# Performance work log

Measured on AMD Instinct MI355X. Metric: run time of the kernel, lower is better.

The kernel has to match this reference:

```python
import jax, jax.numpy as jnp
import numpy as np

TEMP = 1.75   # temp_schedule(epoch=5, warmup=10): 2.5 - 1.5*0.5
ALPHA = 0.5   # blend_schedule(epoch=5): 0.2 + 0.6*0.5
EPS = 1e-5
HEADS = 2


def _ln(x, g, b):
    mu = x.mean(-1, keepdims=True)
    var = ((x - mu) ** 2).mean(-1, keepdims=True)
    return (x - mu) * jax.lax.rsqrt(var + EPS) * g + b


def _gelu(x):
    return jax.nn.gelu(x, approximate=False)  # torch nn.GELU default = exact erf


def _attn_pool(x, ln_g, ln_b, in_w, in_b, out_w, out_b):
    # x: [N, T, E]; nn.MultiheadAttention self-attention then mean over T
    N, T, E = x.shape
    Dh = E // HEADS
    xn = _ln(x, ln_g, ln_b)
    qkv = xn @ in_w + in_b                      # [N, T, 3E] (in_w stored [E, 3E])
    q, k, v = jnp.split(qkv, 3, axis=-1)
    q = q.reshape(N, T, HEADS, Dh).transpose(0, 2, 1, 3)
    k = k.reshape(N, T, HEADS, Dh).transpose(0, 2, 1, 3)
    v = v.reshape(N, T, HEADS, Dh).transpose(0, 2, 1, 3)
    scores = jnp.einsum('nhqd,nhkd->nhqk', q, k) / jnp.sqrt(jnp.float32(Dh))
    a = jax.nn.softmax(scores, axis=-1)
    o = jnp.einsum('nhqk,nhkd->nhqd', a, v).transpose(0, 2, 1, 3).reshape(N, T, E)
    o = o @ out_w + out_b                       # [N, T, E]
    return o.mean(axis=1)                       # [N, E]


def setup_inputs() -> dict:
    key = jax.random.key(0)
    ks = iter(jax.random.split(key, 40))
    B, L, T, D = 4, 24, 400, 1024
    H = D // 2  # 512
    G = 4       # groups
    s = 0.02
    r = lambda shp: jax.random.normal(next(ks), shp, dtype=jnp.float32) * s
    inp = {
        'x': jax.random.normal(next(ks), (B, L, T, D), dtype=jnp.float32),
        'mlp_alpha': jnp.ones((L,), jnp.float32),
        # shared MLP: LN -> Linear(D,H) -> GELU -> Linear(H,H)
        's_ln_g': jnp.ones((D,), jnp.float32), 's_ln_b': jnp.zeros((D,), jnp.float32),
        's_w1': r((D, H)), 's_b1': jnp.zeros((H,), jnp.float32),
        's_w2': r((H, H)), 's_b2': jnp.zeros((H,), jnp.float32),
        # 4 group MLPs (stacked)
        'g_ln_g': jnp.ones((G, D), jnp.float32), 'g_ln_b': jnp.zeros((G, D), jnp.float32),
        'g_w1': r((G, D, H)), 'g_b1': jnp.zeros((G, H), jnp.float32),
        'g_w2': r((G, H, H)), 'g_b2': jnp.zeros((G, H), jnp.float32),
        # TimeAttentionPool (shared module): LN + MHA(512, 2 heads) + out_proj
        'p_ln_g': jnp.ones((H,), jnp.float32), 'p_ln_b': jnp.zeros((H,), jnp.float32),
        'p_in_w': r((H, 3 * H)), 'p_in_b': jnp.zeros((3 * H,), jnp.float32),
        'p_out_w': r((H, H)), 'p_out_b': jnp.zeros((H,), jnp.float32),
        # router: Linear(512,128) -> GELU -> Linear(128,1) -> sigmoid(/temp)
        'r_w1': r((H, 128)), 'r_b1': jnp.zeros((128,), jnp.float32),
        'r_w2': r((128, 1)), 'r_b2': jnp.zeros((1,), jnp.float32),
        # post norms
        'pn_g': jnp.ones((H,), jnp.float32), 'pn_b': jnp.zeros((H,), jnp.float32),
        'pnf_g': jnp.ones((H,), jnp.float32), 'pnf_b': jnp.zeros((H,), jnp.float32),
        # classifier 512 -> 256 -> 128 -> 2
        'c_w1': r((H, H // 2)), 'c_b1': jnp.zeros((H // 2,), jnp.float32),
        'c_w2': r((H // 2, H // 4)), 'c_b2': jnp.zeros((H // 4,), jnp.float32),
        'c_w3': r((H // 4, 2)), 'c_b3': jnp.zeros((2,), jnp.float32),
    }
    return inp


def reference(x, mlp_alpha, s_ln_g, s_ln_b, s_w1, s_b1, s_w2, s_b2,
              g_ln_g, g_ln_b, g_w1, g_b1, g_w2, g_b2,
              p_ln_g, p_ln_b, p_in_w, p_in_b, p_out_w, p_out_b,
              r_w1, r_b1, r_w2, r_b2, pn_g, pn_b, pnf_g, pnf_b,
              c_w1, c_b1, c_w2, c_b2, c_w3, c_b3):
    B, L, T, D = x.shape
    G = g_w1.shape[0]
    S = L // G  # group_size = 6; expert i uses group i // S
    H = s_w1.shape[1]

    # shared MLP over all experts at once (dropout inactive in eval)
    xs = _ln(x, s_ln_g, s_ln_b)                              # [B,L,T,D]
    shared = _gelu(xs @ s_w1 + s_b1) @ s_w2 + s_b2           # [B,L,T,H]

    # group MLPs: experts i//S -> group; reshape L -> (G, S)
    xg = x.reshape(B, G, S, T, D)
    xgn = _ln(xg, g_ln_g[:, None, None, :], g_ln_b[:, None, None, :])
    hg = _gelu(jnp.einsum('bgstd,gdh->bgsth', xgn, g_w1) + g_b1[None, :, None, None, :])
    grp = jnp.einsum('bgsth,ghk->bgstk', hg, g_w2) + g_b2[None, :, None, None, :]
    grp = grp.reshape(B, L, T, H)

    weighted = shared + mlp_alpha[None, :, None, None] * grp  # [B,L,T,H]

    # attn-pool every expert stream (fold L into batch)
    time_pooled = _attn_pool(weighted.reshape(B * L, T, H),
                             p_ln_g, p_ln_b, p_in_w, p_in_b, p_out_w, p_out_b)
    time_pooled = time_pooled.reshape(B, L, H)               # [B,L,H]

    # router
    rh = _gelu(time_pooled @ r_w1 + r_b1)
    logits_r = (rh @ r_w2 + r_b2)[..., 0]                    # [B,L]
    learned = jax.nn.sigmoid(logits_r / TEMP)
    routing_weights = ALPHA * learned + (1.0 - ALPHA) / L

    # soft fusion over experts
    fusion = (weighted * routing_weights[:, :, None, None]).sum(axis=1)  # [B,T,H]
    fusion = _ln(fusion, pn_g, pn_b).mean(axis=1)            # [B,H]

    shared_mean = shared.mean(axis=1)                        # [B,T,H]
    time_ctx = _attn_pool(shared_mean, p_ln_g, p_ln_b, p_in_w, p_in_b, p_out_w, p_out_b)

    fused_all = _ln(fusion, pnf_g, pnf_b) + _ln(time_ctx, pnf_g, pnf_b)  # [B,H]

    h = _gelu(fused_all @ c_w1 + c_b1)
    h = _gelu(h @ c_w2 + c_b2)
    logits = h @ c_w3 + c_b3                                 # [B,2]
    return logits, routing_weights, fused_all, time_pooled
```

## Files before the change

### kernel.cpp

```cpp
#include <hip/hip_runtime.h>
#include <stdint.h>


typedef float f32x4 __attribute__((ext_vector_type(4)));
typedef short bf16x8 __attribute__((ext_vector_type(8)));

__device__ __forceinline__ float bf2f(unsigned short u) {
  return __uint_as_float(((unsigned int)u) << 16);
}
__device__ __forceinline__ unsigned short f2bf(float f) {
  unsigned int u = __float_as_uint(f);
  u += 0x7fffu + ((u >> 16) & 1u);
  return (unsigned short)(u >> 16);
}
__device__ __forceinline__ float erf_fast(float x) {
  const float ax = fabsf(x);
  const float t = 1.0f / fmaf(0.3275911f, ax, 1.0f);
  float p = fmaf(1.061405429f, t, -1.453152027f);
  p = fmaf(p, t, 1.421413741f);
  p = fmaf(p, t, -0.284496736f);
  p = fmaf(p, t, 0.254829592f);
  const float e = __expf(-ax * ax);
  const float r = 1.0f - p * t * e;
  return copysignf(r, x);
}
__device__ __forceinline__ float gelu_f(float x) {
  return 0.5f * x * (1.0f + erf_fast(x * 0.70710678118654752440f));
}

typedef __attribute__((address_space(1))) const unsigned int gas_u32;
typedef __attribute__((address_space(3))) unsigned int las_u32;
__device__ __forceinline__ void gload16(const unsigned short* g, unsigned short* l) {
  __builtin_amdgcn_global_load_lds((gas_u32*)g, (las_u32*)l, 16, 0, 0);
}

template <int EPI, int GROUPED>
__global__ __launch_bounds__(256, 4) void gemm_bt(
    const unsigned short* __restrict__ A, const unsigned short* __restrict__ WT,
    const float* __restrict__ bias, unsigned short* __restrict__ Cout,
    const unsigned short* __restrict__ WT2, const float* __restrict__ bias2,
    const float* __restrict__ alpha_vec, unsigned short* __restrict__ vtbuf, int K,
    int N, int ldout, int Mslice) {
  const int tid = (int)threadIdx.x;
  const int w = tid >> 6, lane = tid & 63, g = lane >> 4, ql = lane & 15;
  const int wr = w >> 1, wc = w & 1;

  int bm, bn, z = 0;
  if (!GROUPED) {
    const int nbm = (int)gridDim.x, nbn = (int)gridDim.y;
    const int nb = nbm * nbn;
    const int lin = (int)blockIdx.x + nbm * (int)blockIdx.y;
    const int q = nb >> 3, r8 = nb & 7;
    const int xcd = lin & 7, c = lin >> 3;
    const int base = (xcd < r8) ? xcd * (q + 1) : r8 * (q + 1) + (xcd - r8) * q;
    const int widx = base + c;
    bm = widx / nbn;
    bn = widx - bm * nbn;
  } else {
    const int nbm = (int)gridDim.x, nbn = (int)gridDim.y;
    const int per_z = nbm * nbn;
    const int nb = per_z * (int)gridDim.z;
    const int lin =
        (int)blockIdx.x + nbm * ((int)blockIdx.y + (int)gridDim.y * (int)blockIdx.z);
    const int q = nb >> 3, r8 = nb & 7;
    const int xcd = lin & 7, c = lin >> 3;
    const int base = (xcd < r8) ? xcd * (q + 1) : r8 * (q + 1) + (xcd - r8) * q;
    const int widx = base + c;
    z = widx / per_z;
    const int rem = widx - z * per_z;
    bm = rem / nbn;
    bn = rem - bm * nbn;
  }
  const int n0 = bn * 128;

  int rowbase, rows_here;
  int nw0 = n0;
  const unsigned short* wt = WT;
  const float* bs = bias;
  if (GROUPED) {
    const int grp = z & 3;
    rowbase = z * Mslice + bm * 128;
    rows_here = Mslice - bm * 128;
    if (rows_here > 128) rows_here = 128;
    if (EPI == 4) {
      if (bn >= 4) {
        wt = WT2 + (size_t)grp * 512 * (size_t)K;
        bs = bias2 + (size_t)grp * 512;
        nw0 = n0 - 512;
      }
    } else if (EPI == 5) {
      wt = WT + (size_t)grp * (size_t)N * (size_t)K;
    } else {
      wt = WT + (size_t)grp * (size_t)N * (size_t)K;
      bs = bias + (size_t)grp * (size_t)N;
    }
  } else {
    rowbase = bm * 128;
    rows_here = Mslice - bm * 128;
    if (rows_here > 128) rows_here = 128;
  }

  __shared__ __align__(16) unsigned short sA[2][128 * 32];
  __shared__ __align__(16) unsigned short sB[2][128 * 32];

  f32x4 acc[4][4];
#pragma unroll
  for (int i = 0; i < 4; ++i)
#pragma unroll
    for (int j = 0; j < 4; ++j) acc[i][j] = (f32x4){0.f, 0.f, 0.f, 0.f};

  const int swzg = (lane & 3) ^ ((lane >> 3) & 3);
  const int rA0 = w * 32 + (lane >> 2);
  const int rA1 = rA0 + 16;
  const int rA0c = rA0 < rows_here ? rA0 : rows_here - 1;
  const int rA1c = rA1 < rows_here ? rA1 : rows_here - 1;
  const unsigned short* a0p = A + (size_t)(rowbase + rA0c) * K + swzg * 8;
  const unsigned short* a1p = A + (size_t)(rowbase + rA1c) * K + swzg * 8;
  const unsigned short* b0p = wt + (size_t)(nw0 + rA0) * K + swzg * 8;
  const unsigned short* b1p = wt + (size_t)(nw0 + rA1) * K + swzg * 8;
  const int ldsw = w * 1024;

  const int aroff = (wr * 64 + ql) * 32 + ((g ^ ((ql >> 1) & 3)) * 8);
  const int broff = (wc * 64 + ql) * 32 + ((g ^ ((ql >> 1) & 3)) * 8);

  const int nsteps = K >> 5;
  gload16(a0p, &sA[0][ldsw]);
  gload16(a1p, &sA[0][ldsw + 512]);
  gload16(b0p, &sB[0][ldsw]);
  gload16(b1p, &sB[0][ldsw + 512]);
  __syncthreads();

  for (int s = 0; s < nsteps; ++s) {
    const int cur = s & 1;
    if (s + 1 < nsteps) {
      const int k0 = (s + 1) << 5;
      const int nxt = cur ^ 1;
      gload16(a0p + k0, &sA[nxt][ldsw]);
      gload16(a1p + k0, &sA[nxt][ldsw + 512]);
      gload16(b0p + k0, &sB[nxt][ldsw]);
      gload16(b1p + k0, &sB[nxt][ldsw + 512]);
    }
    bf16x8 af[4], bfr[4];
#pragma unroll
    for (int mi = 0; mi < 4; ++mi)
      af[mi] = *(const bf16x8*)(&sA[cur][aroff + mi * 512]);
#pragma unroll
    for (int ni = 0; ni < 4; ++ni)
      bfr[ni] = *(const bf16x8*)(&sB[cur][broff + ni * 512]);
#pragma unroll
    for (int mi = 0; mi < 4; ++mi)
#pragma unroll
      for (int ni = 0; ni < 4; ++ni)
        acc[mi][ni] =
            __builtin_amdgcn_mfma_f32_16x16x32_bf16(af[mi], bfr[ni], acc[mi][ni], 0, 0, 0);
    __syncthreads();
  }

#pragma unroll
  for (int mi = 0; mi < 4; ++mi) {
#pragma unroll
    for (int r = 0; r < 4; ++r) {
      const int rloc = wr * 64 + mi * 16 + 4 * g + r;
      if (rloc >= rows_here) continue;
      const int grow = rowbase + rloc;
      float alpha_r = 1.f;
      float mu_r = 0.f, rstd_r = 1.f;
      const float* b2row = bias2;
      if (GROUPED && (EPI == 4 || EPI == 5)) {
        const int l_idx = (grow / 400) % 24;
        if (EPI == 5) b2row = bias2 + (size_t)l_idx * 512;
        if (EPI == 4) alpha_r = alpha_vec[l_idx];
      }
      if (EPI == 6) {
        const float2 strow = ((const float2*)bias2)[grow];
        mu_r = strow.x;
        rstd_r = strow.y;
      }
#pragma unroll
      for (int ni = 0; ni < 4; ++ni) {
        const int col = n0 + wc * 64 + ni * 16 + ql;
        const int colw = (EPI == 4 && bn >= 4) ? (col - 512) : col;
        float v;
        if (EPI == 5) {
          v = acc[mi][ni][r] + b2row[col];
        } else if (EPI == 6) {
          v = rstd_r * acc[mi][ni][r] + (bs[col] - rstd_r * mu_r * alpha_vec[col]);
        } else {
          v = acc[mi][ni][r] + bs[colw];
        }
        if (EPI == 1 || EPI == 4) v = gelu_f(v);
        if (EPI == 4 && bn >= 4) v *= alpha_r;
        if (EPI == 3 || EPI == 6) {
          if (col < 1024) {
            Cout[(size_t)grow * ldout + col] = f2bf(v);
          } else {
            vtbuf[(size_t)grow * 512 + (col - 1024)] = f2bf(v);
          }
        } else {
          Cout[(size_t)grow * ldout + col] = f2bf(v);
        }
      }
    }
  }
}

__global__ void transpose_v(const unsigned short* __restrict__ vbuf,
                            unsigned short* __restrict__ vt) {
  const int p = blockIdx.z;
  const int h = p & 1, nst = p >> 1;
  const int t0 = blockIdx.x * 32, d0 = blockIdx.y * 32;
  __shared__ unsigned short tile[32][33];
  const int tx = threadIdx.x, ty = threadIdx.y;
#pragma unroll
  for (int i = 0; i < 4; ++i) {
    const int t = t0 + ty + i * 8;
    if (t < 400)
      tile[ty + i * 8][tx] = vbuf[((size_t)nst * 400 + t) * 512 + h * 256 + d0 + tx];
  }
  __syncthreads();
  const int t = t0 + tx;
  if (t < 400) {
#pragma unroll
    for (int i = 0; i < 4; ++i)
      vt[((size_t)p * 256 + d0 + ty + i * 8) * 400 + t] = tile[tx][ty + i * 8];
  }
}

__global__ __launch_bounds__(256, 2) void attn_fwd(const unsigned short* __restrict__ qk,
                                                   const unsigned short* __restrict__ vt,
                                                   float* __restrict__ pool_part) {
  const int nb = (int)gridDim.x;
  int flat = (int)blockIdx.x;
  flat = (flat & 7) * (nb >> 3) + (flat >> 3);
  const int qt = flat % 7;
  const int h = (flat / 7) & 1;
  const int n = flat / 14;
  const int q0 = qt * 64;

  const int tid = (int)threadIdx.x;
  const int w = tid >> 6, lane = tid & 63, g = lane >> 4, ql = lane & 15;

  __shared__ __align__(16) unsigned short slab[400 * 32];
  __shared__ __align__(16) unsigned short Pc[4][512];
  __shared__ float rs[4][16];
  __shared__ float psum[4][256];

  const int qr = q0 + w * 16 + ql;
  const int qrc = qr < 400 ? qr : 399;
  const unsigned short* qp = qk + ((size_t)n * 400 + qrc) * 1024 + h * 256 + g * 8;
  bf16x8 qf[8];
#pragma unroll
  for (int d0 = 0; d0 < 8; ++d0) qf[d0] = *(const bf16x8*)(qp + d0 * 32);

  f32x4 st[25];
#pragma unroll
  for (int kf = 0; kf < 25; ++kf) st[kf] = (f32x4){0.f, 0.f, 0.f, 0.f};

  const unsigned short* kbase = qk + (size_t)n * 400 * 1024 + 512 + h * 256;
  for (int d0 = 0; d0 < 8; ++d0) {
    bf16x8 stg[7];
#pragma unroll
    for (int c = 0; c < 7; ++c) {
      const int q = tid + c * 256;
      const int r = q >> 2, slot = q & 3;
      if (r < 400)
        stg[c] = *(const bf16x8*)(kbase + (size_t)r * 1024 + d0 * 32 + slot * 8);
    }
    __syncthreads();
#pragma unroll
    for (int c = 0; c < 7; ++c) {
      const int q = tid + c * 256;
      const int r = q >> 2, slot = q & 3;
      if (r < 400) *(bf16x8*)(slab + r * 32 + (slot ^ ((r >> 1) & 3)) * 8) = stg[c];
    }
    __syncthreads();
#pragma unroll
    for (int kf = 0; kf < 25; ++kf) {
      const int r = kf * 16 + ql;
      bf16x8 kfr = *(const bf16x8*)(slab + r * 32 + ((g ^ ((r >> 1) & 3)) * 8));
      st[kf] = __builtin_amdgcn_mfma_f32_16x16x32_bf16(kfr, qf[d0], st[kf], 0, 0, 0);
    }
  }

  const float sc = 0.0625f;
  float m = -3.0e38f;
#pragma unroll
  for (int kf = 0; kf < 25; ++kf)
    m = fmaxf(m, fmaxf(fmaxf(st[kf][0], st[kf][1]), fmaxf(st[kf][2], st[kf][3])));
  m = fmaxf(m, __shfl_xor(m, 16));
  m = fmaxf(m, __shfl_xor(m, 32));
  float sum = 0.f;
  uint2 pp[25];
#pragma unroll
  for (int kf = 0; kf < 25; ++kf) {
    float e0 = __expf((st[kf][0] - m) * sc);
    float e1 = __expf((st[kf][1] - m) * sc);
    float e2 = __expf((st[kf][2] - m) * sc);
    float e3 = __expf((st[kf][3] - m) * sc);
    sum += (e0 + e1) + (e2 + e3);
    pp[kf].x = (unsigned int)f2bf(e0) | ((unsigned int)f2bf(e1) << 16);
    pp[kf].y = (unsigned int)f2bf(e2) | ((unsigned int)f2bf(e3) << 16);
  }
  sum += __shfl_xor(sum, 16);
  sum += __shfl_xor(sum, 32);
  if (g == 0) rs[w][ql] = sum;

  f32x4 oacc[16];
#pragma unroll
  for (int nf = 0; nf < 16; ++nf) oacc[nf] = (f32x4){0.f, 0.f, 0.f, 0.f};

  unsigned short* Pw = Pc[w];
  const unsigned short* vbase = vt + (size_t)(n * 2 + h) * 256 * 400;
  for (int kt = 0; kt < 13; ++kt) {
    const int k0 = kt * 32;
    bf16x8 stg[4];
#pragma unroll
    for (int c = 0; c < 4; ++c) {
      const int q = tid + c * 256;
      const int r = q >> 2, slot = q & 3;
      int kc = k0 + slot * 8;
      if (kc >= 400) kc = 0;
      stg[c] = *(const bf16x8*)(vbase + (size_t)r * 400 + kc);
    }
    __syncthreads();
#pragma unroll
    for (int c = 0; c < 4; ++c) {
      const int q = tid + c * 256;
      const int r = q >> 2, slot = q & 3;
      *(bf16x8*)(slab + r * 32 + (slot ^ ((r >> 1) & 3)) * 8) = stg[c];
    }
    {
      const int kf0 = 2 * kt;
      *(uint2*)(Pw + ql * 32 + 4 * g) = pp[kf0];
      uint2 hi = (kf0 + 1 < 25) ? pp[kf0 + 1] : (uint2){0u, 0u};
      *(uint2*)(Pw + ql * 32 + 16 + 4 * g) = hi;
    }
    __syncthreads();
    bf16x8 pa = *(const bf16x8*)(Pw + ql * 32 + g * 8);
#pragma unroll
    for (int nf = 0; nf < 16; ++nf) {
      const int r = nf * 16 + ql;
      bf16x8 vb = *(const bf16x8*)(slab + r * 32 + ((g ^ ((r >> 1) & 3)) * 8));
      oacc[nf] = __builtin_amdgcn_mfma_f32_16x16x32_bf16(pa, vb, oacc[nf], 0, 0, 0);
    }
  }

  const float inv0 = 1.f / rs[w][4 * g + 0];
  const float inv1 = 1.f / rs[w][4 * g + 1];
  const float inv2 = 1.f / rs[w][4 * g + 2];
  const float inv3 = 1.f / rs[w][4 * g + 3];

#pragma unroll
  for (int nf = 0; nf < 16; ++nf) {
    float s = 0.f;
#pragma unroll
    for (int r = 0; r < 4; ++r) {
      const int qrow = q0 + w * 16 + 4 * g + r;
      const float invr = (r == 0) ? inv0 : (r == 1) ? inv1 : (r == 2) ? inv2 : inv3;
      if (qrow < 400) s += oacc[nf][r] * invr;
    }
    s += __shfl_xor(s, 16);
    s += __shfl_xor(s, 32);
    if (lane < 16) psum[w][nf * 16 + ql] = s;
  }
  __syncthreads();
  if (tid < 256) {
    const float s = psum[0][tid] + psum[1][tid] + psum[2][tid] + psum[3][tid];
    pool_part[((size_t)((n * 2 + h) * 7 + qt)) * 256 + tid] = s;
  }
}

__global__ void pool_fin(const float* __restrict__ part, float* __restrict__ out,
                         int Ns) {
  const int i = (int)blockIdx.x * 256 + (int)threadIdx.x;
  if (i >= Ns * 512) return;
  const int n = i >> 9, c = i & 511;
  const int h = c >> 8, d = c & 255;
  float s = 0.f;
#pragma unroll
  for (int qt = 0; qt < 7; ++qt)
    s += part[((size_t)((n * 2 + h) * 7 + qt)) * 256 + d];
  out[i] = s * (1.f / 400.f);
}

__global__ void row_stats(const unsigned short* __restrict__ in,
                          float2* __restrict__ st) {
  const int row = (int)blockIdx.x;
  const int t = (int)threadIdx.x;
  ushort4 v = ((const ushort4*)in)[(size_t)row * 128 + t];
  const float x0 = bf2f(v.x), x1 = bf2f(v.y), x2 = bf2f(v.z), x3 = bf2f(v.w);
  float s1 = x0 + x1 + x2 + x3;
  float s2 = x0 * x0 + x1 * x1 + x2 * x2 + x3 * x3;
  for (int mlane = 1; mlane < 64; mlane <<= 1) {
    s1 += __shfl_xor(s1, mlane);
    s2 += __shfl_xor(s2, mlane);
  }
  __shared__ float red[4];
  if ((t & 63) == 0) {
    red[t >> 6] = s1;
    red[2 + (t >> 6)] = s2;
  }
  __syncthreads();
  if (t == 0) {
    s1 = red[0] + red[1];
    s2 = red[2] + red[3];
    const float mu = s1 * (1.f / 512.f);
    const float var = s2 * (1.f / 512.f) - mu * mu;
    st[row] = make_float2(mu, rsqrtf(var + 1e-5f));
  }
}

__global__ void row_sum_bf16(const unsigned short* __restrict__ wm,
                             float* __restrict__ out, int K) {
  const int wid = (int)blockIdx.x * 4 + ((int)threadIdx.x >> 6);
  const int lane = (int)threadIdx.x & 63;
  float s = 0.f;
  for (int k = lane; k < K; k += 64) s += bf2f(wm[(size_t)wid * K + k]);
#pragma unroll
  for (int d = 1; d < 64; d <<= 1) s += __shfl_xor(s, d);
  if (lane == 0) out[wid] = s;
}

template <int TIN, int TOUT>
__global__ void ln_rows(const void* __restrict__ inv, void* __restrict__ outv,
                        const float* __restrict__ gam, const float* __restrict__ bet,
                        int C) {
  const int row = blockIdx.x, t = (int)threadIdx.x;
  float x0, x1, x2, x3;
  if (TIN == 0) {
    float4 v = ((const float4*)inv)[(size_t)row * (C >> 2) + t];
    x0 = v.x; x1 = v.y; x2 = v.z; x3 = v.w;
  } else {
    ushort4 v = ((const ushort4*)inv)[(size_t)row * (C >> 2) + t];
    x0 = bf2f(v.x); x1 = bf2f(v.y); x2 = bf2f(v.z); x3 = bf2f(v.w);
  }
  float s1 = x0 + x1 + x2 + x3;
  float s2 = x0 * x0 + x1 * x1 + x2 * x2 + x3 * x3;
  for (int mlane = 1; mlane < 64; mlane <<= 1) {
    s1 += __shfl_xor(s1, mlane);
    s2 += __shfl_xor(s2, mlane);
  }
  __shared__ float red[8];
  const int nw = blockDim.x >> 6;
  if ((t & 63) == 0) {
    red[t >> 6] = s1;
    red[4 + (t >> 6)] = s2;
  }
  __syncthreads();
  s1 = 0.f; s2 = 0.f;
  for (int i = 0; i < nw; ++i) {
    s1 += red[i];
    s2 += red[4 + i];
  }
  const float mu = s1 / C;
  const float var = s2 / C - mu * mu;
  const float rstd = rsqrtf(var + 1e-5f);
  float y0 = (x0 - mu) * rstd, y1 = (x1 - mu) * rstd, y2 = (x2 - mu) * rstd,
        y3 = (x3 - mu) * rstd;
  if (gam) {
    const int c = t * 4;
    y0 = y0 * gam[c + 0] + bet[c + 0];
    y1 = y1 * gam[c + 1] + bet[c + 1];
    y2 = y2 * gam[c + 2] + bet[c + 2];
    y3 = y3 * gam[c + 3] + bet[c + 3];
  }
  if (TOUT == 0) {
    ushort4 o;
    o.x = f2bf(y0); o.y = f2bf(y1); o.z = f2bf(y2); o.w = f2bf(y3);
    ((ushort4*)outv)[(size_t)row * (C >> 2) + t] = o;
  } else {
    float4 o;
    o.x = y0; o.y = y1; o.z = y2; o.w = y3;
    ((float4*)outv)[(size_t)row * (C >> 2) + t] = o;
  }
}

__global__ void transpose_w(const float* __restrict__ W, const float* __restrict__ scale,
                            unsigned short* __restrict__ WT, int K, int N) {
  __shared__ float tile[32][33];
  const int k0 = blockIdx.x * 32, n0 = blockIdx.y * 32, zg = blockIdx.z;
  const float* Wz = W + (size_t)zg * K * N;
  const float* sz = scale ? scale + (size_t)zg * K : (const float*)0;
  unsigned short* WTz = WT + (size_t)zg * (size_t)K * N;
  const int tx = threadIdx.x, ty = threadIdx.y;
#pragma unroll
  for (int i = 0; i < 4; ++i)
    tile[ty + i * 8][tx] = Wz[(size_t)(k0 + ty + i * 8) * N + n0 + tx];
  __syncthreads();
#pragma unroll
  for (int i = 0; i < 4; ++i) {
    const int nn = n0 + ty + i * 8;
    const int kk = k0 + tx;
    float v = tile[tx][ty + i * 8];
    if (sz) v *= sz[kk];
    WTz[(size_t)nn * K + kk] = f2bf(v);
  }
}

__global__ void transpose_wf(const float* __restrict__ W, float* __restrict__ WT, int K,
                             int N) {
  __shared__ float tile[32][33];
  const int k0 = blockIdx.x * 32, n0 = blockIdx.y * 32;
  const int tx = threadIdx.x, ty = threadIdx.y;
#pragma unroll
  for (int i = 0; i < 4; ++i) {
    const int k = k0 + ty + i * 8;
    if (k < K && n0 + tx < N) tile[ty + i * 8][tx] = W[(size_t)k * N + n0 + tx];
  }
  __syncthreads();
#pragma unroll
  for (int i = 0; i < 4; ++i) {
    const int nn = n0 + ty + i * 8;
    const int kk = k0 + tx;
    if (nn < N && kk < K) WT[(size_t)nn * K + kk] = tile[tx][ty + i * 8];
  }
}

__global__ void build_wcomb2(const unsigned short* __restrict__ sw2T,
                             const unsigned short* __restrict__ gw2T,
                             unsigned short* __restrict__ wc) {
  const int q = (int)blockIdx.x * 256 + (int)threadIdx.x;
  if (q >= 4 * 512 * 256) return;
  const int grp = q / (512 * 256);
  const int rem = q - grp * (512 * 256);
  const int n = rem >> 8, kq = rem & 255;
  ushort4 v;
  if (kq < 128) {
    v = ((const ushort4*)sw2T)[(size_t)n * 128 + kq];
  } else {
    v = ((const ushort4*)gw2T)[((size_t)grp * 512 + n) * 128 + (kq - 128)];
  }
  ((ushort4*)wc)[q] = v;
}

__global__ void build_beff2(const float* __restrict__ s_b2, const float* __restrict__ g_b2,
                            const float* __restrict__ alpha, float* __restrict__ beff2) {
  const int l = (int)blockIdx.x;
  const int n = (int)threadIdx.x;
  beff2[(size_t)l * 512 + n] = s_b2[n] + alpha[l] * g_b2[(size_t)(l / 6) * 512 + n];
}

#define BF_KC 64
__global__ void bias_fold_part(const float* __restrict__ W, const float* __restrict__ lb,
                               float* __restrict__ part, int K, int N) {
  const int zg = blockIdx.z;
  const int n = blockIdx.x * 256 + (int)threadIdx.x;
  const int kc = blockIdx.y;
  const int kpc = K / BF_KC;
  const float* Wz = W + (size_t)zg * K * N;
  const float* lbz = lb + (size_t)zg * K;
  float acc = 0.f;
  const int k1 = (kc + 1) * kpc;
  for (int k = kc * kpc; k < k1; ++k) acc += lbz[k] * Wz[(size_t)k * N + n];
  part[((size_t)zg * BF_KC + kc) * N + n] = acc;
}
__global__ void bias_fold_final(const float* __restrict__ part, const float* __restrict__ b,
                                float* __restrict__ beff, int N) {
  const int zg = blockIdx.y;
  const int n = blockIdx.x * 256 + (int)threadIdx.x;
  float acc = b[(size_t)zg * N + n];
#pragma unroll
  for (int c = 0; c < BF_KC; ++c) acc += part[((size_t)zg * BF_KC + c) * N + n];
  beff[(size_t)zg * N + n] = acc;
}

__global__ void mean_h(const unsigned short* __restrict__ h,
                       unsigned short* __restrict__ out) {
  const int i = blockIdx.x * 256 + (int)threadIdx.x;
  if (i >= 4 * 400 * 128) return;
  const int b = i / (400 * 128);
  const int rem = i - b * (400 * 128);
  const int t = rem >> 7, c4 = rem & 127;
  float a0 = 0.f, a1 = 0.f, a2 = 0.f, a3 = 0.f;
  for (int l = 0; l < 24; ++l) {
    ushort4 v = *(const ushort4*)(h + ((size_t)(b * 24 + l) * 400 + t) * 1024 + c4 * 4);
    a0 += bf2f(v.x); a1 += bf2f(v.y); a2 += bf2f(v.z); a3 += bf2f(v.w);
  }
  ushort4 o;
  o.x = f2bf(a0 * (1.f / 24.f));
  o.y = f2bf(a1 * (1.f / 24.f));
  o.z = f2bf(a2 * (1.f / 24.f));
  o.w = f2bf(a3 * (1.f / 24.f));
  *(ushort4*)(out + ((size_t)(b * 400 + t)) * 512 + c4 * 4) = o;
}

template <int TIN>
__global__ void mean_t_part(const void* __restrict__ inv, float* __restrict__ part,
                            int Ns) {
  const int bx = (int)blockIdx.x;
  const int n = bx >> 2, cb = bx & 3;
  const int p = (int)blockIdx.y;
  const int c = cb * 128 + (int)threadIdx.x;
  float acc = 0.f;
  const int t0 = p * 50;
  if (TIN) {
    const unsigned short* in = (const unsigned short*)inv;
    for (int t = t0; t < t0 + 50; ++t) acc += bf2f(in[((size_t)n * 400 + t) * 512 + c]);
  } else {
    const float* in = (const float*)inv;
    for (int t = t0; t < t0 + 50; ++t) acc += in[((size_t)n * 400 + t) * 512 + c];
  }
  part[((size_t)p * Ns + n) * 512 + c] = acc;
}
__global__ void mean_t_fin(const float* __restrict__ part, float* __restrict__ out,
                           int Ns) {
  const int i = (int)blockIdx.x * 256 + (int)threadIdx.x;
  if (i >= Ns * 512) return;
  const int n = i >> 9, c = i & 511;
  float acc = 0.f;
#pragma unroll
  for (int p = 0; p < 8; ++p) acc += part[((size_t)p * Ns + n) * 512 + c];
  out[i] = acc * (1.f / 400.f);
}

__global__ void fuse_ln(const unsigned short* __restrict__ wgt,
                        const float* __restrict__ rw, const float* __restrict__ gam,
                        const float* __restrict__ bet, float* __restrict__ fln) {
  const int row = (int)blockIdx.x;
  const int b = row / 400, tt = row - b * 400;
  const int t = (int)threadIdx.x;
  float a0 = 0.f, a1 = 0.f, a2 = 0.f, a3 = 0.f;
  for (int l = 0; l < 24; ++l) {
    const float wv = rw[b * 24 + l];
    ushort4 v = *(const ushort4*)(wgt + ((size_t)(b * 24 + l) * 400 + tt) * 512 + t * 4);
    a0 += wv * bf2f(v.x); a1 += wv * bf2f(v.y);
    a2 += wv * bf2f(v.z); a3 += wv * bf2f(v.w);
  }
  float s1 = a0 + a1 + a2 + a3;
  float s2 = a0 * a0 + a1 * a1 + a2 * a2 + a3 * a3;
  for (int mlane = 1; mlane < 64; mlane <<= 1) {
    s1 += __shfl_xor(s1, mlane);
    s2 += __shfl_xor(s2, mlane);
  }
  __shared__ float red[4];
  if ((t & 63) == 0) {
    red[t >> 6] = s1;
    red[2 + (t >> 6)] = s2;
  }
  __syncthreads();
  s1 = red[0] + red[1];
  s2 = red[2] + red[3];
  const float mu = s1 * (1.f / 512.f);
  const float var = s2 * (1.f / 512.f) - mu * mu;
  const float rstd = rsqrtf(var + 1e-5f);
  const int c = t * 4;
  float4 o;
  o.x = (a0 - mu) * rstd * gam[c + 0] + bet[c + 0];
  o.y = (a1 - mu) * rstd * gam[c + 1] + bet[c + 1];
  o.z = (a2 - mu) * rstd * gam[c + 2] + bet[c + 2];
  o.w = (a3 - mu) * rstd * gam[c + 3] + bet[c + 3];
  ((float4*)fln)[(size_t)row * 128 + t] = o;
}

__global__ void ln2_add(const float* __restrict__ a, const float* __restrict__ bsrc,
                        const float* __restrict__ gam, const float* __restrict__ bet,
                        float* __restrict__ o1, float* __restrict__ o2) {
  const int row = (int)blockIdx.x;
  const int t = (int)threadIdx.x;
  float4 av = ((const float4*)a)[(size_t)row * 128 + t];
  float4 bv = ((const float4*)bsrc)[(size_t)row * 128 + t];
  float s1a = av.x + av.y + av.z + av.w;
  float s2a = av.x * av.x + av.y * av.y + av.z * av.z + av.w * av.w;
  float s1b = bv.x + bv.y + bv.z + bv.w;
  float s2b = bv.x * bv.x + bv.y * bv.y + bv.z * bv.z + bv.w * bv.w;
  for (int mlane = 1; mlane < 64; mlane <<= 1) {
    s1a += __shfl_xor(s1a, mlane);
    s2a += __shfl_xor(s2a, mlane);
    s1b += __shfl_xor(s1b, mlane);
    s2b += __shfl_xor(s2b, mlane);
  }
  __shared__ float red[8];
  if ((t & 63) == 0) {
    const int wv = t >> 6;
    red[wv] = s1a; red[2 + wv] = s2a; red[4 + wv] = s1b; red[6 + wv] = s2b;
  }
  __syncthreads();
  s1a = red[0] + red[1]; s2a = red[2] + red[3];
  s1b = red[4] + red[5]; s2b = red[6] + red[7];
  const float mua = s1a * (1.f / 512.f);
  const float ra = rsqrtf(s2a * (1.f / 512.f) - mua * mua + 1e-5f);
  const float mub = s1b * (1.f / 512.f);
  const float rb = rsqrtf(s2b * (1.f / 512.f) - mub * mub + 1e-5f);
  const int c = t * 4;
  float4 o;
  o.x = ((av.x - mua) * ra * gam[c + 0] + bet[c + 0]) +
        ((bv.x - mub) * rb * gam[c + 0] + bet[c + 0]);
  o.y = ((av.y - mua) * ra * gam[c + 1] + bet[c + 1]) +
        ((bv.y - mub) * rb * gam[c + 1] + bet[c + 1]);
  o.z = ((av.z - mua) * ra * gam[c + 2] + bet[c + 2]) +
        ((bv.z - mub) * rb * gam[c + 2] + bet[c + 2]);
  o.w = ((av.w - mua) * ra * gam[c + 3] + bet[c + 3]) +
        ((bv.w - mub) * rb * gam[c + 3] + bet[c + 3]);
  ((float4*)o1)[(size_t)row * 128 + t] = o;
  ((float4*)o2)[(size_t)row * 128 + t] = o;
}

template <int WLAYOUT>
__global__ void gemv_wave(const float* __restrict__ A, const float* __restrict__ Wm,
                          const float* __restrict__ b, float* __restrict__ C, int M, int K,
                          int N, int act) {
  const int wid = (int)(blockIdx.x * (blockDim.x >> 6)) + ((int)threadIdx.x >> 6);
  const int lane = (int)threadIdx.x & 63;
  if (wid >= M * N) return;
  const int row = wid / N, col = wid - row * N;
  const float* a = A + (size_t)row * K;
  float acc = 0.f;
  if (WLAYOUT) {
    const float* wt = Wm + (size_t)col * K;
    for (int k = lane; k < K; k += 64) acc += a[k] * wt[k];
  } else {
    for (int k = lane; k < K; k += 64) acc += a[k] * Wm[(size_t)k * N + col];
  }
#pragma unroll
  for (int d = 1; d < 64; d <<= 1) acc += __shfl_xor(acc, d);
  if (lane == 0) {
    acc += b[col];
    if (act) acc = gelu_f(acc);
    C[wid] = acc;
  }
}

__global__ void routing_k(const float* __restrict__ lr, float* __restrict__ o1,
                          float* __restrict__ o2) {
  const int i = (int)threadIdx.x;
  if (i < 96) {
    const float v = 0.5f / (1.f + __expf(-lr[i] * (1.f / 1.75f))) + (0.5f / 24.f);
    o1[i] = v;
    o2[i] = v;
  }
}

extern "C" void kernel_launch(void* const* d_in, const int* in_sizes, int n_in,
                              void* d_out, int out_size, void* d_ws, size_t ws_size,
                              hipStream_t stream) {
  const float* x = (const float*)d_in[0];
  const float* mlp_alpha = (const float*)d_in[1];
  const float* s_ln_g = (const float*)d_in[2];
  const float* s_ln_b = (const float*)d_in[3];
  const float* s_w1 = (const float*)d_in[4];
  const float* s_b1 = (const float*)d_in[5];
  const float* s_w2 = (const float*)d_in[6];
  const float* s_b2 = (const float*)d_in[7];
  const float* g_ln_g = (const float*)d_in[8];
  const float* g_ln_b = (const float*)d_in[9];
  const float* g_w1 = (const float*)d_in[10];
  const float* g_b1 = (const float*)d_in[11];
  const float* g_w2 = (const float*)d_in[12];
  const float* g_b2 = (const float*)d_in[13];
  const float* p_ln_g = (const float*)d_in[14];
  const float* p_ln_b = (const float*)d_in[15];
  const float* p_in_w = (const float*)d_in[16];
  const float* p_in_b = (const float*)d_in[17];
  const float* p_out_w = (const float*)d_in[18];
  const float* p_out_b = (const float*)d_in[19];
  const float* r_w1 = (const float*)d_in[20];
  const float* r_b1 = (const float*)d_in[21];
  const float* r_w2 = (const float*)d_in[22];
  const float* r_b2 = (const float*)d_in[23];
  const float* pn_g = (const float*)d_in[24];
  const float* pn_b = (const float*)d_in[25];
  const float* pnf_g = (const float*)d_in[26];
  const float* pnf_b = (const float*)d_in[27];
  const float* c_w1 = (const float*)d_in[28];
  const float* c_b1 = (const float*)d_in[29];
  const float* c_w2 = (const float*)d_in[30];
  const float* c_b2 = (const float*)d_in[31];
  const float* c_w3 = (const float*)d_in[32];
  const float* c_b3 = (const float*)d_in[33];

  float* out = (float*)d_out;
  uint8_t* ws = (uint8_t*)d_ws;

  size_t off = 0;
  auto alloc = [&](size_t bytes) -> size_t {
    size_t o = off;
    off += (bytes + 255) & ~(size_t)255;
    return o;
  };
  const size_t off_xhat = alloc(38400ull * 1024 * 2);
  const size_t off_h = alloc(38400ull * 1024 * 2);
  const size_t off_weighted = alloc(38400ull * 512 * 2);
  const size_t off_qk = alloc(38400ull * 1024 * 2);
  const size_t off_pooled = alloc(96ull * 512 * 4);
  const size_t off_rh = alloc(96ull * 128 * 4);
  const size_t off_lr = alloc(96ull * 4);
  const size_t off_rw = alloc(96ull * 4);
  const size_t off_hmean = alloc(1600ull * 512 * 2);
  const size_t off_smb = alloc(1600ull * 512 * 2);
  const size_t off_wn2 = alloc(1600ull * 512 * 2);
  const size_t off_qk2 = alloc(1600ull * 1024 * 2);
  const size_t off_vbuf2 = alloc(1600ull * 512 * 2);
  const size_t off_vt2 = alloc(4ull * 2 * 256 * 400 * 2);
  const size_t off_pooled2 = alloc(4ull * 512 * 4);
  const size_t off_tctx = alloc(4ull * 512 * 4);
  const size_t off_fln = alloc(4ull * 400 * 512 * 4);
  const size_t off_fvec = alloc(4ull * 512 * 4);
  const size_t off_fall = alloc(4ull * 512 * 4);
  const size_t off_c1 = alloc(4ull * 256 * 4);
  const size_t off_c2 = alloc(4ull * 128 * 4);
  const size_t off_sw1T = alloc(512ull * 1024 * 2);
  const size_t off_sw2T = alloc(512ull * 512 * 2);
  const size_t off_gw1T = alloc(4ull * 512 * 1024 * 2);
  const size_t off_gw2T = alloc(4ull * 512 * 512 * 2);
  const size_t off_pinT = alloc(1536ull * 512 * 2);
  const size_t off_wc2 = alloc(4ull * 512 * 1024 * 2);
  const size_t off_sb1e = alloc(512ull * 4);
  const size_t off_gb1e = alloc(4ull * 512 * 4);
  const size_t off_pinbe = alloc(1536ull * 4);
  const size_t off_beff2 = alloc(24ull * 512 * 4);
  const size_t off_bfp_s = alloc((size_t)BF_KC * 512 * 4);
  const size_t off_bfp_g = alloc(4ull * BF_KC * 512 * 4);
  const size_t off_bfp_p = alloc((size_t)BF_KC * 1536 * 4);
  const size_t off_powT = alloc(512ull * 512 * 4);
  const size_t off_rw1T = alloc(128ull * 512 * 4);
  const size_t off_cw1T = alloc(256ull * 512 * 4);
  const size_t off_cw2T = alloc(128ull * 256 * 4);
  const size_t off_mtp = alloc(8ull * 96 * 512 * 4);
  const size_t off_wstats = alloc(38400ull * 8);
  const size_t off_csp = alloc(1536ull * 4);
  const size_t off_pp1 = alloc(96ull * 14 * 256 * 4);
  const size_t off_pp2 = alloc(4ull * 14 * 256 * 4);
  const size_t off_vbuf = off_xhat + 38400ull * 512 * 2;
  const size_t off_vt = off_h + 38400ull * 512 * 2;
  if (off > ws_size) return;

  unsigned short* xhat = (unsigned short*)(ws + off_xhat);
  unsigned short* hbuf = (unsigned short*)(ws + off_h);
  unsigned short* weighted = (unsigned short*)(ws + off_weighted);
  unsigned short* qk = (unsigned short*)(ws + off_qk);
  unsigned short* vbuf = (unsigned short*)(ws + off_vbuf);
  unsigned short* vt = (unsigned short*)(ws + off_vt);
  float* pooled = (float*)(ws + off_pooled);
  float* rh = (float*)(ws + off_rh);
  float* lr = (float*)(ws + off_lr);
  float* rw = (float*)(ws + off_rw);
  unsigned short* hmean_b = (unsigned short*)(ws + off_hmean);
  unsigned short* smean_b = (unsigned short*)(ws + off_smb);
  unsigned short* wn2 = (unsigned short*)(ws + off_wn2);
  unsigned short* qk2 = (unsigned short*)(ws + off_qk2);
  unsigned short* vbuf2 = (unsigned short*)(ws + off_vbuf2);
  unsigned short* vt2 = (unsigned short*)(ws + off_vt2);
  float* pooled2 = (float*)(ws + off_pooled2);
  float* tctx = (float*)(ws + off_tctx);
  float* fln = (float*)(ws + off_fln);
  float* fvec = (float*)(ws + off_fvec);
  float* fall = (float*)(ws + off_fall);
  float* c1 = (float*)(ws + off_c1);
  float* c2 = (float*)(ws + off_c2);
  unsigned short* sw1T = (unsigned short*)(ws + off_sw1T);
  unsigned short* sw2T = (unsigned short*)(ws + off_sw2T);
  unsigned short* gw1T = (unsigned short*)(ws + off_gw1T);
  unsigned short* gw2T = (unsigned short*)(ws + off_gw2T);
  unsigned short* pinT = (unsigned short*)(ws + off_pinT);
  unsigned short* wcomb2 = (unsigned short*)(ws + off_wc2);
  float* sb1e = (float*)(ws + off_sb1e);
  float* gb1e = (float*)(ws + off_gb1e);
  float* pinbe = (float*)(ws + off_pinbe);
  float* beff2 = (float*)(ws + off_beff2);
  float* bfp_s = (float*)(ws + off_bfp_s);
  float* bfp_g = (float*)(ws + off_bfp_g);
  float* bfp_p = (float*)(ws + off_bfp_p);
  float* powT = (float*)(ws + off_powT);
  float* rw1T = (float*)(ws + off_rw1T);
  float* cw1T = (float*)(ws + off_cw1T);
  float* cw2T = (float*)(ws + off_cw2T);
  float* mtp = (float*)(ws + off_mtp);
  float2* wstats = (float2*)(ws + off_wstats);
  float* csP = (float*)(ws + off_csp);
  float* pp1 = (float*)(ws + off_pp1);
  float* pp2 = (float*)(ws + off_pp2);

  transpose_w<<<dim3(32, 16, 1), dim3(32, 8), 0, stream>>>(s_w1, s_ln_g, sw1T, 1024, 512);
  transpose_w<<<dim3(16, 16, 1), dim3(32, 8), 0, stream>>>(s_w2, (const float*)0, sw2T, 512, 512);
  transpose_w<<<dim3(32, 16, 4), dim3(32, 8), 0, stream>>>(g_w1, g_ln_g, gw1T, 1024, 512);
  transpose_w<<<dim3(16, 16, 4), dim3(32, 8), 0, stream>>>(g_w2, (const float*)0, gw2T, 512, 512);
  transpose_w<<<dim3(16, 48, 1), dim3(32, 8), 0, stream>>>(p_in_w, p_ln_g, pinT, 512, 1536);
  transpose_wf<<<dim3(16, 16), dim3(32, 8), 0, stream>>>(p_out_w, powT, 512, 512);
  transpose_wf<<<dim3(16, 4), dim3(32, 8), 0, stream>>>(r_w1, rw1T, 512, 128);
  transpose_wf<<<dim3(16, 8), dim3(32, 8), 0, stream>>>(c_w1, cw1T, 512, 256);
  transpose_wf<<<dim3(8, 4), dim3(32, 8), 0, stream>>>(c_w2, cw2T, 256, 128);
  build_wcomb2<<<2048, 256, 0, stream>>>(sw2T, gw2T, wcomb2);
  build_beff2<<<24, 512, 0, stream>>>(s_b2, g_b2, mlp_alpha, beff2);
  row_sum_bf16<<<384, 256, 0, stream>>>(pinT, csP, 512);
  bias_fold_part<<<dim3(2, BF_KC, 1), 256, 0, stream>>>(s_w1, s_ln_b, bfp_s, 1024, 512);
  bias_fold_final<<<dim3(2, 1), 256, 0, stream>>>(bfp_s, s_b1, sb1e, 512);
  bias_fold_part<<<dim3(2, BF_KC, 4), 256, 0, stream>>>(g_w1, g_ln_b, bfp_g, 1024, 512);
  bias_fold_final<<<dim3(2, 4), 256, 0, stream>>>(bfp_g, g_b1, gb1e, 512);
  bias_fold_part<<<dim3(6, BF_KC, 1), 256, 0, stream>>>(p_in_w, p_ln_b, bfp_p, 512, 1536);
  bias_fold_final<<<dim3(6, 1), 256, 0, stream>>>(bfp_p, p_in_b, pinbe, 1536);

  ln_rows<0, 0><<<38400, 256, 0, stream>>>(x, xhat, (const float*)0, (const float*)0, 1024);

  gemm_bt<4, 1><<<dim3(19, 8, 16), 256, 0, stream>>>(xhat, sw1T, sb1e, hbuf, gw1T, gb1e,
      mlp_alpha, (unsigned short*)0, 1024, 1024, 1024, 2400);

  gemm_bt<5, 1><<<dim3(19, 4, 16), 256, 0, stream>>>(hbuf, wcomb2, (const float*)0,
      weighted, (const unsigned short*)0, beff2, (const float*)0, (unsigned short*)0,
      1024, 512, 512, 2400);

  mean_h<<<800, 256, 0, stream>>>(hbuf, hmean_b);
  gemm_bt<0, 0><<<dim3(13, 4, 1), 256, 0, stream>>>(hmean_b, sw2T, s_b2, smean_b,
      (const unsigned short*)0, (const float*)0, (const float*)0, (unsigned short*)0,
      512, 512, 512, 1600);

  row_stats<<<38400, 128, 0, stream>>>(weighted, wstats);
  gemm_bt<6, 0><<<dim3(300, 12, 1), 256, 0, stream>>>(weighted, pinT, pinbe, qk,
      (const unsigned short*)0, (const float*)wstats, csP, vbuf, 512, 1536, 1024,
      38400);
  transpose_v<<<dim3(13, 8, 192), dim3(32, 8), 0, stream>>>(vbuf, vt);
  attn_fwd<<<dim3(14 * 96), 256, 0, stream>>>(qk, vt, pp1);
  pool_fin<<<192, 256, 0, stream>>>(pp1, pooled, 96);
  gemv_wave<1><<<12288, 256, 0, stream>>>(pooled, powT, p_out_b, out + 2152, 96, 512, 512, 0);

  gemv_wave<1><<<3072, 256, 0, stream>>>(out + 2152, rw1T, r_b1, rh, 96, 512, 128, 1);
  gemv_wave<0><<<24, 256, 0, stream>>>(rh, r_w2, r_b2, lr, 96, 128, 1, 0);
  routing_k<<<1, 128, 0, stream>>>(lr, out + 8, rw);

  fuse_ln<<<1600, 128, 0, stream>>>(weighted, rw, pn_g, pn_b, fln);
  mean_t_part<0><<<dim3(4 * 4, 8), 128, 0, stream>>>(fln, mtp, 4);
  mean_t_fin<<<8, 256, 0, stream>>>(mtp, fvec, 4);

  ln_rows<1, 0><<<1600, 128, 0, stream>>>(smean_b, wn2, (const float*)0, (const float*)0, 512);
  gemm_bt<3, 0><<<dim3(13, 12, 1), 256, 0, stream>>>(wn2, pinT, pinbe, qk2,
      (const unsigned short*)0, (const float*)0, (const float*)0, vbuf2, 512, 1536, 1024,
      1600);
  transpose_v<<<dim3(13, 8, 8), dim3(32, 8), 0, stream>>>(vbuf2, vt2);
  attn_fwd<<<dim3(14 * 4), 256, 0, stream>>>(qk2, vt2, pp2);
  pool_fin<<<8, 256, 0, stream>>>(pp2, pooled2, 4);
  gemv_wave<1><<<512, 256, 0, stream>>>(pooled2, powT, p_out_b, tctx, 4, 512, 512, 0);

  ln2_add<<<4, 128, 0, stream>>>(fvec, tctx, pnf_g, pnf_b, out + 104, fall);

  gemv_wave<1><<<256, 256, 0, stream>>>(fall, cw1T, c_b1, c1, 4, 512, 256, 1);
  gemv_wave<1><<<128, 256, 0, stream>>>(c1, cw2T, c_b2, c2, 4, 256, 128, 1);
  gemv_wave<0><<<2, 256, 0, stream>>>(c2, c_w3, c_b3, out, 4, 128, 2, 0);
}
```

Before: 720.8 us.

## Fuse router tail and classifier chain, raise MFMA wave priority in attention

The router's second GEMV is merged with the sigmoid routing step into one kernel. The final LayerNorm-add and the three classifier GEMVs are merged into a single 512-thread block that keeps intermediates in shared memory. Together these remove several tiny launches and global round-trips. Separately, s_setprio is raised around the MFMA loops in attention so matrix work is favoured over loads from other waves. The single-block classifier does per-thread serial dot products over 512 and 256 elements with uncoalesced weight reads, so it may run slower than the earlier spread-out GEMVs.

After: 789.9 us. +9.6%, slower.

```diff
diff --git a/kernel.cpp b/kernel.cpp
--- a/kernel.cpp
+++ b/kernel.cpp
@@ -274,12 +274,14 @@
       if (r < 400) *(bf16x8*)(slab + r * 32 + (slot ^ ((r >> 1) & 3)) * 8) = stg[c];
     }
     __syncthreads();
+    __builtin_amdgcn_s_setprio(1);
 #pragma unroll
     for (int kf = 0; kf < 25; ++kf) {
       const int r = kf * 16 + ql;
       bf16x8 kfr = *(const bf16x8*)(slab + r * 32 + ((g ^ ((r >> 1) & 3)) * 8));
       st[kf] = __builtin_amdgcn_mfma_f32_16x16x32_bf16(kfr, qf[d0], st[kf], 0, 0, 0);
     }
+    __builtin_amdgcn_s_setprio(0);
   }
 
   const float sc = 0.0625f;
@@ -337,12 +339,14 @@
     }
     __syncthreads();
     bf16x8 pa = *(const bf16x8*)(Pw + ql * 32 + g * 8);
+    __builtin_amdgcn_s_setprio(1);
 #pragma unroll
     for (int nf = 0; nf < 16; ++nf) {
       const int r = nf * 16 + ql;
       bf16x8 vb = *(const bf16x8*)(slab + r * 32 + ((g ^ ((r >> 1) & 3)) * 8));
       oacc[nf] = __builtin_amdgcn_mfma_f32_16x16x32_bf16(pa, vb, oacc[nf], 0, 0, 0);
     }
+    __builtin_amdgcn_s_setprio(0);
   }
 
   const float inv0 = 1.f / rs[w][4 * g + 0];
@@ -652,13 +656,42 @@
   ((float4*)fln)[(size_t)row * 128 + t] = o;
 }
 
-__global__ void ln2_add(const float* __restrict__ a, const float* __restrict__ bsrc,
-                        const float* __restrict__ gam, const float* __restrict__ bet,
-                        float* __restrict__ o1, float* __restrict__ o2) {
-  const int row = (int)blockIdx.x;
+__global__ void router_gemv(const float* __restrict__ rh, const float* __restrict__ w2,
+                            const float* __restrict__ b2, float* __restrict__ o1,
+                            float* __restrict__ o2) {
+  const int wid = (int)blockIdx.x * 4 + ((int)threadIdx.x >> 6);
+  const int lane = (int)threadIdx.x & 63;
+  if (wid >= 96) return;
+  float acc = 0.f;
+  for (int k = lane; k < 128; k += 64) acc += rh[(size_t)wid * 128 + k] * w2[k];
+#pragma unroll
+  for (int d = 1; d < 64; d <<= 1) acc += __shfl_xor(acc, d);
+  if (lane == 0) {
+    const float lrv = acc + b2[0];
+    const float v = 0.5f / (1.f + __expf(-lrv * (1.f / 1.75f))) + (0.5f / 24.f);
+    o1[wid] = v;
+    o2[wid] = v;
+  }
+}
+
+__global__ __launch_bounds__(512) void final_chain(
+    const float* __restrict__ fvec, const float* __restrict__ tctx,
+    const float* __restrict__ gam, const float* __restrict__ bet,
+    const float* __restrict__ cw1T, const float* __restrict__ c_b1,
+    const float* __restrict__ cw2T, const float* __restrict__ c_b2,
+    const float* __restrict__ c_w3, const float* __restrict__ c_b3,
+    float* __restrict__ out) {
+  __shared__ float fall_s[4][512];
+  __shared__ float c1_s[4][256];
+  __shared__ float c2_s[4][128];
+  __shared__ float redA[8], redB[8], redC[8], redD[8];
   const int t = (int)threadIdx.x;
-  float4 av = ((const float4*)a)[(size_t)row * 128 + t];
-  float4 bv = ((const float4*)bsrc)[(size_t)row * 128 + t];
+  const int row = t >> 7;
+  const int q = t & 127;
+  const int wv = t >> 6;
+
+  float4 av = ((const float4*)fvec)[(size_t)row * 128 + q];
+  float4 bv = ((const float4*)tctx)[(size_t)row * 128 + q];
   float s1a = av.x + av.y + av.z + av.w;
   float s2a = av.x * av.x + av.y * av.y + av.z * av.z + av.w * av.w;
   float s1b = bv.x + bv.y + bv.z + bv.w;
@@ -669,19 +702,19 @@
     s1b += __shfl_xor(s1b, mlane);
     s2b += __shfl_xor(s2b, mlane);
   }
-  __shared__ float red[8];
   if ((t & 63) == 0) {
-    const int wv = t >> 6;
-    red[wv] = s1a; red[2 + wv] = s2a; red[4 + wv] = s1b; red[6 + wv] = s2b;
-  }
-  __syncthreads();
-  s1a = red[0] + red[1]; s2a = red[2] + red[3];
-  s1b = red[4] + red[5]; s2b = red[6] + red[7];
+    redA[wv] = s1a; redB[wv] = s2a; redC[wv] = s1b; redD[wv] = s2b;
+  }
+  __syncthreads();
+  s1a = redA[2 * row] + redA[2 * row + 1];
+  s2a = redB[2 * row] + redB[2 * row + 1];
+  s1b = redC[2 * row] + redC[2 * row + 1];
+  s2b = redD[2 * row] + redD[2 * row + 1];
   const float mua = s1a * (1.f / 512.f);
   const float ra = rsqrtf(s2a * (1.f / 512.f) - mua * mua + 1e-5f);
   const float mub = s1b * (1.f / 512.f);
   const float rb = rsqrtf(s2b * (1.f / 512.f) - mub * mub + 1e-5f);
-  const int c = t * 4;
+  const int c = q * 4;
   float4 o;
   o.x = ((av.x - mua) * ra * gam[c + 0] + bet[c + 0]) +
         ((bv.x - mub) * rb * gam[c + 0] + bet[c + 0]);
@@ -691,8 +724,39 @@
         ((bv.z - mub) * rb * gam[c + 2] + bet[c + 2]);
   o.w = ((av.w - mua) * ra * gam[c + 3] + bet[c + 3]) +
         ((bv.w - mub) * rb * gam[c + 3] + bet[c + 3]);
-  ((float4*)o1)[(size_t)row * 128 + t] = o;
-  ((float4*)o2)[(size_t)row * 128 + t] = o;
+  fall_s[row][c + 0] = o.x;
+  fall_s[row][c + 1] = o.y;
+  fall_s[row][c + 2] = o.z;
+  fall_s[row][c + 3] = o.w;
+  ((float4*)(out + 104))[(size_t)row * 128 + q] = o;
+  __syncthreads();
+
+#pragma unroll
+  for (int half = 0; half < 2; ++half) {
+    const int oidx = t + half * 512;
+    const int i = oidx >> 8, j = oidx & 255;
+    float acc = c_b1[j];
+    const float* wrow = cw1T + (size_t)j * 512;
+    for (int k = 0; k < 512; ++k) acc += fall_s[i][k] * wrow[k];
+    c1_s[i][j] = gelu_f(acc);
+  }
+  __syncthreads();
+
+  {
+    const int i = t >> 7, j = t & 127;
+    float acc = c_b2[j];
+    const float* wrow = cw2T + (size_t)j * 256;
+    for (int k = 0; k < 256; ++k) acc += c1_s[i][k] * wrow[k];
+    c2_s[i][j] = gelu_f(acc);
+  }
+  __syncthreads();
+
+  if (t < 8) {
+    const int i = t >> 1, j = t & 1;
+    float acc = c_b3[j];
+    for (int k = 0; k < 128; ++k) acc += c2_s[i][k] * c_w3[k * 2 + j];
+    out[i * 2 + j] = acc;
+  }
 }
 
 template <int WLAYOUT>
@@ -717,16 +781,6 @@
     acc += b[col];
     if (act) acc = gelu_f(acc);
     C[wid] = acc;
-  }
-}
-
-__global__ void routing_k(const float* __restrict__ lr, float* __restrict__ o1,
-                          float* __restrict__ o2) {
-  const int i = (int)threadIdx.x;
-  if (i < 96) {
-    const float v = 0.5f / (1.f + __expf(-lr[i] * (1.f / 1.75f))) + (0.5f / 24.f);
-    o1[i] = v;
-    o2[i] = v;
   }
 }
 
@@ -783,7 +837,6 @@
   const size_t off_qk = alloc(38400ull * 1024 * 2);
   const size_t off_pooled = alloc(96ull * 512 * 4);
   const size_t off_rh = alloc(96ull * 128 * 4);
-  const size_t off_lr = alloc(96ull * 4);
   const size_t off_rw = alloc(96ull * 4);
   const size_t off_hmean = alloc(1600ull * 512 * 2);
   const size_t off_smb = alloc(1600ull * 512 * 2);
@@ -795,9 +848,6 @@
   const size_t off_tctx = alloc(4ull * 512 * 4);
   const size_t off_fln = alloc(4ull * 400 * 512 * 4);
   const size_t off_fvec = alloc(4ull * 512 * 4);
-  const size_t off_fall = alloc(4ull * 512 * 4);
-  const size_t off_c1 = alloc(4ull * 256 * 4);
-  const size_t off_c2 = alloc(4ull * 128 * 4);
   const size_t off_sw1T = alloc(512ull * 1024 * 2);
   const size_t off_sw2T = alloc(512ull * 512 * 2);
   const size_t off_gw1T = alloc(4ull * 512 * 1024 * 2);
@@ -832,7 +882,6 @@
   unsigned short* vt = (unsigned short*)(ws + off_vt);
   float* pooled = (float*)(ws + off_pooled);
   float* rh = (float*)(ws + off_rh);
-  float* lr = (float*)(ws + off_lr);
   float* rw = (float*)(ws + off_rw);
   unsigned short* hmean_b = (unsigned short*)(ws + off_hmean);
   unsigned short* smean_b = (unsigned short*)(ws + off_smb);
@@ -844,9 +893,6 @@
   float* tctx = (float*)(ws + off_tctx);
   float* fln = (float*)(ws + off_fln);
   float* fvec = (float*)(ws + off_fvec);
-  float* fall = (float*)(ws + off_fall);
-  float* c1 = (float*)(ws + off_c1);
-  float* c2 = (float*)(ws + off_c2);
   unsigned short* sw1T = (unsigned short*)(ws + off_sw1T);
   unsigned short* sw2T = (unsigned short*)(ws + off_sw2T);
   unsigned short* gw1T = (unsigned short*)(ws + off_gw1T);
@@ -913,8 +959,7 @@
   gemv_wave<1><<<12288, 256, 0, stream>>>(pooled, powT, p_out_b, out + 2152, 96, 512, 512, 0);
 
   gemv_wave<1><<<3072, 256, 0, stream>>>(out + 2152, rw1T, r_b1, rh, 96, 512, 128, 1);
-  gemv_wave<0><<<24, 256, 0, stream>>>(rh, r_w2, r_b2, lr, 96, 128, 1, 0);
-  routing_k<<<1, 128, 0, stream>>>(lr, out + 8, rw);
+  router_gemv<<<24, 256, 0, stream>>>(rh, r_w2, r_b2, out + 8, rw);
 
   fuse_ln<<<1600, 128, 0, stream>>>(weighted, rw, pn_g, pn_b, fln);
   mean_t_part<0><<<dim3(4 * 4, 8), 128, 0, stream>>>(fln, mtp, 4);
@@ -929,9 +974,6 @@
   pool_fin<<<8, 256, 0, stream>>>(pp2, pooled2, 4);
   gemv_wave<1><<<512, 256, 0, stream>>>(pooled2, powT, p_out_b, tctx, 4, 512, 512, 0);
 
-  ln2_add<<<4, 128, 0, stream>>>(fvec, tctx, pnf_g, pnf_b, out + 104, fall);
-
-  gemv_wave<1><<<256, 256, 0, stream>>>(fall, cw1T, c_b1, c1, 4, 512, 256, 1);
-  gemv_wave<1><<<128, 256, 0, stream>>>(c1, cw2T, c_b2, c2, 4, 256, 128, 1);
-  gemv_wave<0><<<2, 256, 0, stream>>>(c2, c_w3, c_b3, out, 4, 128, 2, 0);
-}
+  final_chain<<<1, 512, 0, stream>>>(fvec, tctx, pnf_g, pnf_b, cw1T, c_b1, cw2T, c_b2,
+                                     c_w3, c_b3, out);
+}
```
